# Kernel optimization log

Measured on AMD Instinct MI355X. Metric: run time of the kernel, lower is better.

Reference implementation:

```python
import jax, jax.numpy as jnp
import numpy as np

B, S, VOCAB, P, K, R = 64, 512, 50000, 300, 50, 5


def setup_inputs() -> dict:
    key = jax.random.key(0)
    k0, k1, k2, k3, k4, k5, k6 = jax.random.split(key, 7)
    idx = jax.random.randint(k0, (B, S), 0, VOCAB)
    emb = jax.random.normal(k1, (VOCAB, P), dtype=jnp.float32) * 0.02
    emb = emb.at[0].set(0.0)  # padding_idx=0 row is zero
    C = jax.random.normal(k2, (K, P), dtype=jnp.float32)  # label embeddings ~ N(0,1)
    conv_w = jax.random.normal(k3, (1, 1, 1, 2 * R + 1), dtype=jnp.float32) * 0.1
    conv_b = jax.random.normal(k4, (1,), dtype=jnp.float32) * 0.1
    W2 = jax.random.normal(k5, (K, P), dtype=jnp.float32) / np.sqrt(P).astype(np.float32)
    b2 = jax.random.normal(k6, (K,), dtype=jnp.float32) * 0.01
    return {"idx": idx, "emb": emb, "C": C, "conv_w": conv_w, "conv_b": conv_b, "W2": W2, "b2": b2}


def reference(idx, emb, C, conv_w, conv_b, W2, b2):
    # Embed sentence: [B, S, P]
    x = emb[idx]
    # Cosine label attention
    x_hat = x / (jnp.linalg.norm(x, axis=2, keepdims=True) + 0.001)
    l_hat = C / (jnp.linalg.norm(C, axis=1, keepdims=True) + 0.001)
    G_hat = jnp.einsum('kp,bsp->bks', l_hat, x_hat)  # [B, K, S]
    # Pad seq dim by R on both sides, then conv2d(1->1, kernel (1, 2R+1))
    G_pad = jnp.pad(G_hat, ((0, 0), (0, 0), (R, R)))
    m = jax.lax.conv_general_dilated(
        G_pad[:, None, :, :], conv_w, window_strides=(1, 1), padding='VALID',
        dimension_numbers=('NCHW', 'OIHW', 'NCHW'))[:, 0] + conv_b[0]  # [B, K, S]
    m = jax.nn.relu(m)
    m = jnp.max(m, axis=1)  # max over labels -> [B, S]
    beta = jax.nn.softmax(m, axis=1)[..., None]  # [B, S, 1]
    pooled = jnp.mean(beta * x, axis=1)  # [B, P]
    # Dropout is identity in eval mode; final linear P -> K
    return pooled @ W2.T + b2
```

## Files before the change

### kernel.cpp

```cpp
#include <hip/hip_runtime.h>

#define B_   64
#define S_   512
#define P_   300
#define K_   50
#define MPAD 64
#define LDX  344
#define NS   48
#define SCH  32
#define LDM  67

typedef short short8v __attribute__((ext_vector_type(8)));
typedef float float4v __attribute__((ext_vector_type(4)));

__device__ __forceinline__ short f2bf(float f) {
  unsigned u = __builtin_bit_cast(unsigned, f);
  u = (u + 0x7FFFu + ((u >> 16) & 1u)) >> 16;
  return (short)u;
}
__device__ __forceinline__ float bf2f(short h) {
  return __builtin_bit_cast(float, ((unsigned)(unsigned short)h) << 16);
}

__global__ __launch_bounds__(64) void k1_prep(const float* __restrict__ C,
                                              const float* __restrict__ W2,
                                              short* __restrict__ apack) {
  int bid = blockIdx.x;
  int mat = bid / 40;
  int rem = bid - mat * 40;
  int mt  = rem / 10;
  int ks  = rem - mt * 10;
  int lane = threadIdx.x;
  __shared__ float invn[16];
  if (mat == 0) {
    int rl = lane >> 2, q = lane & 3;
    int m = mt * 16 + rl;
    float ss = 0.f;
    if (m < K_) {
      for (int p = q; p < P_; p += 4) { float v = C[m * P_ + p]; ss += v * v; }
    }
    ss += __shfl_xor(ss, 1);
    ss += __shfl_xor(ss, 2);
    if (q == 0) invn[rl] = 1.f / (sqrtf(ss) + 0.001f);
  }
  __syncthreads();
  int ml = lane & 15, quad = lane >> 4;
  int m = mt * 16 + ml;
  const float* src = (mat == 0) ? C : W2;
  short8v v8;
  #pragma unroll
  for (int j = 0; j < 8; ++j) {
    int k = ks * 32 + quad * 8 + j;
    float v = 0.f;
    if (m < K_ && k < P_) {
      v = src[m * P_ + k];
      if (mat == 0) v *= invn[ml];
    }
    v8[j] = f2bf(v);
  }
  *(short8v*)(apack + (size_t)(((mat * 4 + mt) * 10 + ks) * 512 + lane * 8)) = v8;
}

__global__ __launch_bounds__(256, 3) void k2_gemm(const int* __restrict__ idx,
                                                  const float* __restrict__ emb,
                                                  const short* __restrict__ apack,
                                                  short* __restrict__ Yt,
                                                  const float* __restrict__ conv_w,
                                                  const float* __restrict__ conv_b,
                                                  float* __restrict__ mbuf) {
  __shared__ __align__(16) char smem_raw[NS * LDX * 2];
  __shared__ float scale_s[NS];
  __shared__ float mpart[8][SCH];
  short (*xt)[LDX] = (short(*)[LDX])smem_raw;
  float (*gst)[LDM] = (float(*)[LDM])smem_raw;

  int bid = blockIdx.x;
  int b = bid >> 4, s0 = (bid & 15) * SCH;
  int tid = threadIdx.x;
  int lane = tid & 63;
  int wu = __builtin_amdgcn_readfirstlane(tid >> 6);

  int rows[12];
  #pragma unroll
  for (int r = 0; r < 12; ++r) {
    int sg = s0 - 8 + wu * 12 + r;
    int sgc = sg < 0 ? 0 : (sg >= S_ ? S_ - 1 : sg);
    rows[r] = idx[b * S_ + sgc];
  }

  float ssr[12];
  #pragma unroll
  for (int h = 0; h < 2; ++h) {
    float4 va[6], vb[6];
    #pragma unroll
    for (int r = 0; r < 6; ++r) {
      const float4* src = (const float4*)(emb + (size_t)rows[h * 6 + r] * P_);
      va[r] = src[lane];
      if (lane < 11) vb[r] = src[64 + lane];
    }
    #pragma unroll
    for (int r = 0; r < 6; ++r) {
      int ls = wu * 12 + h * 6 + r;
      int sg = s0 - 8 + ls;
      bool oob = (sg < 0) || (sg >= S_);
      float4 v = va[r];
      if (oob) { v.x = 0.f; v.y = 0.f; v.z = 0.f; v.w = 0.f; }
      float ss = v.x * v.x + v.y * v.y + v.z * v.z + v.w * v.w;
      short4 hh; hh.x = f2bf(v.x); hh.y = f2bf(v.y); hh.z = f2bf(v.z); hh.w = f2bf(v.w);
      *(short4*)&xt[ls][4 * lane] = hh;
      if (lane < 11) {
        float4 v2 = vb[r];
        if (oob) { v2.x = 0.f; v2.y = 0.f; v2.z = 0.f; v2.w = 0.f; }
        ss += v2.x * v2.x + v2.y * v2.y + v2.z * v2.z + v2.w * v2.w;
        short4 h2; h2.x = f2bf(v2.x); h2.y = f2bf(v2.y); h2.z = f2bf(v2.z); h2.w = f2bf(v2.w);
        *(short4*)&xt[ls][256 + 4 * lane] = h2;
      } else if (lane < 16) {
        short4 z = {0, 0, 0, 0};
        *(short4*)&xt[ls][300 + 4 * (lane - 11)] = z;
      }
      ssr[h * 6 + r] = ss;
    }
  }
  #pragma unroll
  for (int r = 0; r < 12; ++r) {
    float ss = ssr[r];
    #pragma unroll
    for (int off = 32; off > 0; off >>= 1) ss += __shfl_xor(ss, off);
    if (lane == 0) scale_s[wu * 12 + r] = 1.f / (sqrtf(ss) + 0.001f);
  }

  const short8v* a1p = (const short8v*)(apack) + (size_t)((0 * 4 + wu) * 10) * 64 + lane;
  const short8v* a2p = (const short8v*)(apack) + (size_t)((1 * 4 + wu) * 10) * 64 + lane;
  short8v a1f[10], a2f[10];
  #pragma unroll
  for (int ks = 0; ks < 10; ++ks) { a1f[ks] = a1p[ks * 64]; a2f[ks] = a2p[ks * 64]; }

  __syncthreads();

  float4v accG[3] = {};
  float4v accY[2] = {};
  int ml = lane & 15, quad = lane >> 4;
  #pragma unroll
  for (int ks = 0; ks < 10; ++ks) {
    int kk = ks * 32 + quad * 8;
    #pragma unroll
    for (int nt = 0; nt < 3; ++nt) {
      short8v bg = *(const short8v*)&xt[nt * 16 + ml][kk];
      accG[nt] = __builtin_amdgcn_mfma_f32_16x16x32_bf16(a1f[ks], bg, accG[nt], 0, 0, 0);
    }
    #pragma unroll
    for (int nt = 0; nt < 2; ++nt) {
      short8v by = *(const short8v*)&xt[8 + nt * 16 + ml][kk];
      accY[nt] = __builtin_amdgcn_mfma_f32_16x16x32_bf16(a2f[ks], by, accY[nt], 0, 0, 0);
    }
  }

  #pragma unroll
  for (int nt = 0; nt < 2; ++nt) {
    int sg = s0 + nt * 16 + ml;
    #pragma unroll
    for (int reg = 0; reg < 4; ++reg) {
      int m = wu * 16 + quad * 4 + reg;
      if (m < K_) Yt[(size_t)(b * MPAD + m) * S_ + sg] = f2bf(accY[nt][reg]);
    }
  }

  float wvv[11];
  #pragma unroll
  for (int t = 0; t < 11; ++t) wvv[t] = conv_w[t];
  float cb = conv_b[0];

  __syncthreads();

  #pragma unroll
  for (int nt = 0; nt < 3; ++nt) {
    int scol = nt * 16 + ml;
    float sc = scale_s[scol];
    #pragma unroll
    for (int reg = 0; reg < 4; ++reg) {
      int m = wu * 16 + quad * 4 + reg;
      gst[scol][m] = accG[nt][reg] * sc;
    }
  }
  __syncthreads();

  int sl = tid & 31, kg = tid >> 5;
  float part = 0.f;
  for (int k = kg; k < K_; k += 8) {
    float acc = cb;
    #pragma unroll
    for (int t = 0; t < 11; ++t) acc += wvv[t] * gst[sl + 3 + t][k];
    part = fmaxf(part, fmaxf(acc, 0.f));
  }
  mpart[kg][sl] = part;
  __syncthreads();
  if (tid < SCH) {
    float m0 = mpart[0][tid];
    #pragma unroll
    for (int i = 1; i < 8; ++i) m0 = fmaxf(m0, mpart[i][tid]);
    mbuf[b * S_ + s0 + tid] = m0;
  }
}

__global__ __launch_bounds__(512) void k3_pool(const float* __restrict__ mbuf,
                                               const short* __restrict__ Yt,
                                               const float* __restrict__ b2,
                                               float* __restrict__ out) {
  __shared__ float beta[S_];
  __shared__ float red[8];
  int b = blockIdx.x;
  int tid = threadIdx.x;
  int lane = tid & 63, wv = tid >> 6;

  float mx = mbuf[b * S_ + tid];

  float r = mx;
  #pragma unroll
  for (int off = 32; off > 0; off >>= 1) r = fmaxf(r, __shfl_xor(r, off));
  if (lane == 0) red[wv] = r;
  __syncthreads();
  float bm = red[0];
  #pragma unroll
  for (int i = 1; i < 8; ++i) bm = fmaxf(bm, red[i]);
  float e = __expf(mx - bm);
  r = e;
  #pragma unroll
  for (int off = 32; off > 0; off >>= 1) r += __shfl_xor(r, off);
  __syncthreads();
  if (lane == 0) red[wv] = r;
  __syncthreads();
  float sum = 0.f;
  #pragma unroll
  for (int i = 0; i < 8; ++i) sum += red[i];
  beta[tid] = e / (sum * (float)S_);
  __syncthreads();

  for (int k = wv; k < K_; k += 8) {
    short8v y = *(const short8v*)(Yt + (((size_t)(b * MPAD + k)) << 9) + lane * 8);
    const float4* bp = (const float4*)&beta[lane * 8];
    float4 b0 = bp[0], b1 = bp[1];
    float acc = b0.x * bf2f(y[0]) + b0.y * bf2f(y[1]) +
                b0.z * bf2f(y[2]) + b0.w * bf2f(y[3]) +
                b1.x * bf2f(y[4]) + b1.y * bf2f(y[5]) +
                b1.z * bf2f(y[6]) + b1.w * bf2f(y[7]);
    #pragma unroll
    for (int off = 32; off > 0; off >>= 1) acc += __shfl_xor(acc, off);
    if (lane == 0) out[b * K_ + k] = acc + b2[k];
  }
}

extern "C" void kernel_launch(void* const* d_in, const int* in_sizes, int n_in,
                              void* d_out, int out_size, void* d_ws, size_t ws_size,
                              hipStream_t stream) {
  const int*   idx    = (const int*)  d_in[0];
  const float* emb    = (const float*)d_in[1];
  const float* C      = (const float*)d_in[2];
  const float* conv_w = (const float*)d_in[3];
  const float* conv_b = (const float*)d_in[4];
  const float* W2     = (const float*)d_in[5];
  const float* b2     = (const float*)d_in[6];
  float* out = (float*)d_out;

  char* ws = (char*)d_ws;
  short* apack = (short*)(ws);
  short* Yt    = (short*)(ws + 81920);
  float* mbuf  = (float*)(ws + 81920 + 4194304);

  hipLaunchKernelGGL(k1_prep, dim3(80),   dim3(64),  0, stream, C, W2, apack);
  hipLaunchKernelGGL(k2_gemm, dim3(1024), dim3(256), 0, stream,
                     idx, emb, apack, Yt, conv_w, conv_b, mbuf);
  hipLaunchKernelGGL(k3_pool, dim3(64),   dim3(512), 0, stream, mbuf, Yt, b2, out);
}
```

Baseline: 142.9 us.

## Fuse pooling kernel into GEMM via last-block atomic counter; raise occupancy

Drops the separate softmax/pooling kernel. Each batch row now has an atomic counter, reset in the prep kernel, and the last of its 16 GEMM blocks to finish computes the softmax and the weighted pooling, which saves a kernel launch and its dependency gap. Launch bounds go from 3 to 4 blocks per SM, and A-fragments are loaded inside the k-loop instead of being preloaded, to cut register pressure. The risks are more global-load latency inside the MFMA loop and a serialized tail on the last block of each batch row.

```diff
diff --git a/kernel.cpp b/kernel.cpp
--- a/kernel.cpp
+++ b/kernel.cpp
@@ -24,13 +24,15 @@
 
 __global__ __launch_bounds__(64) void k1_prep(const float* __restrict__ C,
                                               const float* __restrict__ W2,
-                                              short* __restrict__ apack) {
+                                              short* __restrict__ apack,
+                                              unsigned* __restrict__ cnt) {
   int bid = blockIdx.x;
+  int lane = threadIdx.x;
+  if (bid == 0) cnt[lane] = 0u;
   int mat = bid / 40;
   int rem = bid - mat * 40;
   int mt  = rem / 10;
   int ks  = rem - mt * 10;
-  int lane = threadIdx.x;
   __shared__ float invn[16];
   if (mat == 0) {
     int rl = lane >> 2, q = lane & 3;
@@ -61,16 +63,21 @@
   *(short8v*)(apack + (size_t)(((mat * 4 + mt) * 10 + ks) * 512 + lane * 8)) = v8;
 }
 
-__global__ __launch_bounds__(256, 3) void k2_gemm(const int* __restrict__ idx,
+__global__ __launch_bounds__(256, 4) void k2_gemm(const int* __restrict__ idx,
                                                   const float* __restrict__ emb,
                                                   const short* __restrict__ apack,
                                                   short* __restrict__ Yt,
                                                   const float* __restrict__ conv_w,
                                                   const float* __restrict__ conv_b,
-                                                  float* __restrict__ mbuf) {
+                                                  float* __restrict__ mbuf,
+                                                  const float* __restrict__ b2,
+                                                  float* __restrict__ out,
+                                                  unsigned* __restrict__ cnt) {
   __shared__ __align__(16) char smem_raw[NS * LDX * 2];
   __shared__ float scale_s[NS];
   __shared__ float mpart[8][SCH];
+  __shared__ float redf[4];
+  __shared__ int last_s;
   short (*xt)[LDX] = (short(*)[LDX])smem_raw;
   float (*gst)[LDM] = (float(*)[LDM])smem_raw;
 
@@ -128,30 +135,27 @@
     for (int off = 32; off > 0; off >>= 1) ss += __shfl_xor(ss, off);
     if (lane == 0) scale_s[wu * 12 + r] = 1.f / (sqrtf(ss) + 0.001f);
   }
-
-  const short8v* a1p = (const short8v*)(apack) + (size_t)((0 * 4 + wu) * 10) * 64 + lane;
-  const short8v* a2p = (const short8v*)(apack) + (size_t)((1 * 4 + wu) * 10) * 64 + lane;
-  short8v a1f[10], a2f[10];
-  #pragma unroll
-  for (int ks = 0; ks < 10; ++ks) { a1f[ks] = a1p[ks * 64]; a2f[ks] = a2p[ks * 64]; }
-
   __syncthreads();
 
   float4v accG[3] = {};
   float4v accY[2] = {};
   int ml = lane & 15, quad = lane >> 4;
+  const short8v* a1p = (const short8v*)(apack) + (size_t)((0 * 4 + wu) * 10) * 64 + lane;
+  const short8v* a2p = (const short8v*)(apack) + (size_t)((1 * 4 + wu) * 10) * 64 + lane;
   #pragma unroll
   for (int ks = 0; ks < 10; ++ks) {
+    short8v a1 = a1p[ks * 64];
+    short8v a2 = a2p[ks * 64];
     int kk = ks * 32 + quad * 8;
     #pragma unroll
     for (int nt = 0; nt < 3; ++nt) {
       short8v bg = *(const short8v*)&xt[nt * 16 + ml][kk];
-      accG[nt] = __builtin_amdgcn_mfma_f32_16x16x32_bf16(a1f[ks], bg, accG[nt], 0, 0, 0);
+      accG[nt] = __builtin_amdgcn_mfma_f32_16x16x32_bf16(a1, bg, accG[nt], 0, 0, 0);
     }
     #pragma unroll
     for (int nt = 0; nt < 2; ++nt) {
       short8v by = *(const short8v*)&xt[8 + nt * 16 + ml][kk];
-      accY[nt] = __builtin_amdgcn_mfma_f32_16x16x32_bf16(a2f[ks], by, accY[nt], 0, 0, 0);
+      accY[nt] = __builtin_amdgcn_mfma_f32_16x16x32_bf16(a2, by, accY[nt], 0, 0, 0);
     }
   }
 
@@ -200,49 +204,48 @@
     for (int i = 1; i < 8; ++i) m0 = fmaxf(m0, mpart[i][tid]);
     mbuf[b * S_ + s0 + tid] = m0;
   }
-}
-
-__global__ __launch_bounds__(512) void k3_pool(const float* __restrict__ mbuf,
-                                               const short* __restrict__ Yt,
-                                               const float* __restrict__ b2,
-                                               float* __restrict__ out) {
-  __shared__ float beta[S_];
-  __shared__ float red[8];
-  int b = blockIdx.x;
-  int tid = threadIdx.x;
-  int lane = tid & 63, wv = tid >> 6;
-
-  float mx = mbuf[b * S_ + tid];
-
+  __syncthreads();
+  __threadfence();
+  if (tid == 0) {
+    unsigned old = atomicAdd(&cnt[b], 1u);
+    last_s = (old == 15u);
+  }
+  __syncthreads();
+  if (!last_s) return;
+
+  __threadfence();
+  float* beta = (float*)smem_raw;
+  int wv = tid >> 6;
+
+  float m0 = mbuf[b * S_ + tid];
+  float m1 = mbuf[b * S_ + 256 + tid];
+  float mx = fmaxf(m0, m1);
   float r = mx;
   #pragma unroll
   for (int off = 32; off > 0; off >>= 1) r = fmaxf(r, __shfl_xor(r, off));
-  if (lane == 0) red[wv] = r;
-  __syncthreads();
-  float bm = red[0];
-  #pragma unroll
-  for (int i = 1; i < 8; ++i) bm = fmaxf(bm, red[i]);
-  float e = __expf(mx - bm);
-  r = e;
+  if (lane == 0) redf[wv] = r;
+  __syncthreads();
+  float bm = fmaxf(fmaxf(redf[0], redf[1]), fmaxf(redf[2], redf[3]));
+  float e0 = __expf(m0 - bm), e1 = __expf(m1 - bm);
+  r = e0 + e1;
   #pragma unroll
   for (int off = 32; off > 0; off >>= 1) r += __shfl_xor(r, off);
   __syncthreads();
-  if (lane == 0) red[wv] = r;
-  __syncthreads();
-  float sum = 0.f;
-  #pragma unroll
-  for (int i = 0; i < 8; ++i) sum += red[i];
-  beta[tid] = e / (sum * (float)S_);
-  __syncthreads();
-
-  for (int k = wv; k < K_; k += 8) {
+  if (lane == 0) redf[wv] = r;
+  __syncthreads();
+  float inv = 1.f / ((redf[0] + redf[1] + redf[2] + redf[3]) * (float)S_);
+  beta[tid] = e0 * inv;
+  beta[tid + 256] = e1 * inv;
+  __syncthreads();
+
+  float4 bb0 = *(const float4*)&beta[lane * 8];
+  float4 bb1 = *(const float4*)&beta[lane * 8 + 4];
+  for (int k = wv; k < K_; k += 4) {
     short8v y = *(const short8v*)(Yt + (((size_t)(b * MPAD + k)) << 9) + lane * 8);
-    const float4* bp = (const float4*)&beta[lane * 8];
-    float4 b0 = bp[0], b1 = bp[1];
-    float acc = b0.x * bf2f(y[0]) + b0.y * bf2f(y[1]) +
-                b0.z * bf2f(y[2]) + b0.w * bf2f(y[3]) +
-                b1.x * bf2f(y[4]) + b1.y * bf2f(y[5]) +
-                b1.z * bf2f(y[6]) + b1.w * bf2f(y[7]);
+    float acc = bb0.x * bf2f(y[0]) + bb0.y * bf2f(y[1]) +
+                bb0.z * bf2f(y[2]) + bb0.w * bf2f(y[3]) +
+                bb1.x * bf2f(y[4]) + bb1.y * bf2f(y[5]) +
+                bb1.z * bf2f(y[6]) + bb1.w * bf2f(y[7]);
     #pragma unroll
     for (int off = 32; off > 0; off >>= 1) acc += __shfl_xor(acc, off);
     if (lane == 0) out[b * K_ + k] = acc + b2[k];
@@ -262,12 +265,12 @@
   float* out = (float*)d_out;
 
   char* ws = (char*)d_ws;
-  short* apack = (short*)(ws);
-  short* Yt    = (short*)(ws + 81920);
-  float* mbuf  = (float*)(ws + 81920 + 4194304);
-
-  hipLaunchKernelGGL(k1_prep, dim3(80),   dim3(64),  0, stream, C, W2, apack);
+  short*    apack = (short*)(ws);
+  short*    Yt    = (short*)(ws + 81920);
+  float*    mbuf  = (float*)(ws + 81920 + 4194304);
+  unsigned* cnt   = (unsigned*)(ws + 81920 + 4194304 + 131072);
+
+  hipLaunchKernelGGL(k1_prep, dim3(80),   dim3(64),  0, stream, C, W2, apack, cnt);
   hipLaunchKernelGGL(k2_gemm, dim3(1024), dim3(256), 0, stream,
-                     idx, emb, apack, Yt, conv_w, conv_b, mbuf);
-  hipLaunchKernelGGL(k3_pool, dim3(64),   dim3(512), 0, stream, mbuf, Yt, b2, out);
-}
+                     idx, emb, apack, Yt, conv_w, conv_b, mbuf, b2, out, cnt);
+}
```

After: 245.1 us. 1.71x slower.

## Stage embedding rows via direct global-to-LDS loads and split pooling across more blocks

Applied to the files above, without the earlier changes.

The gather of embedding rows in the GEMM kernel now uses global_load_lds DMA straight into shared memory as fp32. The rows are then converted in place to bf16 with packed conversion instructions, and the row norms are computed from LDS. This removes the register round-trip on the gather and lets the A-fragment loads overlap with it. The cost is a larger LDS footprint, so occupancy drops from 3 to 2 blocks per CU. The pooling kernel is also split four ways over labels, giving 256 blocks, and beta is hoisted out of the label loop; each block now recomputes the softmax.

```diff
diff --git a/kernel.cpp b/kernel.cpp
--- a/kernel.cpp
+++ b/kernel.cpp
@@ -5,21 +5,31 @@
 #define P_   300
 #define K_   50
 #define MPAD 64
-#define LDX  344
 #define NS   48
 #define SCH  32
+#define LDB  1232
 #define LDM  67
 
 typedef short short8v __attribute__((ext_vector_type(8)));
 typedef float float4v __attribute__((ext_vector_type(4)));
 
+__device__ __forceinline__ float bf2f(short h) {
+  return __builtin_bit_cast(float, ((unsigned)(unsigned short)h) << 16);
+}
 __device__ __forceinline__ short f2bf(float f) {
   unsigned u = __builtin_bit_cast(unsigned, f);
   u = (u + 0x7FFFu + ((u >> 16) & 1u)) >> 16;
   return (short)u;
 }
-__device__ __forceinline__ float bf2f(short h) {
-  return __builtin_bit_cast(float, ((unsigned)(unsigned short)h) << 16);
+__device__ __forceinline__ unsigned cvtpk(float lo, float hi) {
+  unsigned r;
+  asm("v_cvt_pk_bf16_f32 %0, %1, %2" : "=v"(r) : "v"(lo), "v"(hi));
+  return r;
+}
+__device__ __forceinline__ void dma16(const float* g, void* l) {
+  __builtin_amdgcn_global_load_lds(
+      (const __attribute__((address_space(1))) void*)g,
+      (__attribute__((address_space(3))) void*)l, 16, 0, 0);
 }
 
 __global__ __launch_bounds__(64) void k1_prep(const float* __restrict__ C,
@@ -61,17 +71,16 @@
   *(short8v*)(apack + (size_t)(((mat * 4 + mt) * 10 + ks) * 512 + lane * 8)) = v8;
 }
 
-__global__ __launch_bounds__(256, 3) void k2_gemm(const int* __restrict__ idx,
+__global__ __launch_bounds__(256, 2) void k2_gemm(const int* __restrict__ idx,
                                                   const float* __restrict__ emb,
                                                   const short* __restrict__ apack,
                                                   short* __restrict__ Yt,
                                                   const float* __restrict__ conv_w,
                                                   const float* __restrict__ conv_b,
                                                   float* __restrict__ mbuf) {
-  __shared__ __align__(16) char smem_raw[NS * LDX * 2];
+  __shared__ __align__(16) char smem_raw[NS * LDB];
   __shared__ float scale_s[NS];
   __shared__ float mpart[8][SCH];
-  short (*xt)[LDX] = (short(*)[LDX])smem_raw;
   float (*gst)[LDM] = (float(*)[LDM])smem_raw;
 
   int bid = blockIdx.x;
@@ -88,45 +97,16 @@
     rows[r] = idx[b * S_ + sgc];
   }
 
-  float ssr[12];
-  #pragma unroll
-  for (int h = 0; h < 2; ++h) {
-    float4 va[6], vb[6];
-    #pragma unroll
-    for (int r = 0; r < 6; ++r) {
-      const float4* src = (const float4*)(emb + (size_t)rows[h * 6 + r] * P_);
-      va[r] = src[lane];
-      if (lane < 11) vb[r] = src[64 + lane];
-    }
-    #pragma unroll
-    for (int r = 0; r < 6; ++r) {
-      int ls = wu * 12 + h * 6 + r;
-      int sg = s0 - 8 + ls;
-      bool oob = (sg < 0) || (sg >= S_);
-      float4 v = va[r];
-      if (oob) { v.x = 0.f; v.y = 0.f; v.z = 0.f; v.w = 0.f; }
-      float ss = v.x * v.x + v.y * v.y + v.z * v.z + v.w * v.w;
-      short4 hh; hh.x = f2bf(v.x); hh.y = f2bf(v.y); hh.z = f2bf(v.z); hh.w = f2bf(v.w);
-      *(short4*)&xt[ls][4 * lane] = hh;
-      if (lane < 11) {
-        float4 v2 = vb[r];
-        if (oob) { v2.x = 0.f; v2.y = 0.f; v2.z = 0.f; v2.w = 0.f; }
-        ss += v2.x * v2.x + v2.y * v2.y + v2.z * v2.z + v2.w * v2.w;
-        short4 h2; h2.x = f2bf(v2.x); h2.y = f2bf(v2.y); h2.z = f2bf(v2.z); h2.w = f2bf(v2.w);
-        *(short4*)&xt[ls][256 + 4 * lane] = h2;
-      } else if (lane < 16) {
-        short4 z = {0, 0, 0, 0};
-        *(short4*)&xt[ls][300 + 4 * (lane - 11)] = z;
-      }
-      ssr[h * 6 + r] = ss;
-    }
-  }
   #pragma unroll
   for (int r = 0; r < 12; ++r) {
-    float ss = ssr[r];
-    #pragma unroll
-    for (int off = 32; off > 0; off >>= 1) ss += __shfl_xor(ss, off);
-    if (lane == 0) scale_s[wu * 12 + r] = 1.f / (sqrtf(ss) + 0.001f);
+    int ls = wu * 12 + r;
+    int sg = s0 - 8 + ls;
+    if (sg >= 0 && sg < S_) {
+      const float* src = emb + (size_t)rows[r] * P_;
+      char* dst = smem_raw + ls * LDB;
+      dma16(src + 4 * lane, dst);
+      dma16(src + 44 + 4 * lane, dst + 176);
+    }
   }
 
   const short8v* a1p = (const short8v*)(apack) + (size_t)((0 * 4 + wu) * 10) * 64 + lane;
@@ -135,6 +115,35 @@
   #pragma unroll
   for (int ks = 0; ks < 10; ++ks) { a1f[ks] = a1p[ks * 64]; a2f[ks] = a2p[ks * 64]; }
 
+  asm volatile("s_waitcnt vmcnt(0)" ::: "memory");
+
+  #pragma unroll
+  for (int r = 0; r < 12; ++r) {
+    int ls = wu * 12 + r;
+    int sg = s0 - 8 + ls;
+    char* rowp = smem_raw + ls * LDB;
+    float ss = 0.f;
+    if (sg >= 0 && sg < S_) {
+      float4 va = *(const float4*)(rowp + 16 * lane);
+      float4 vb = {0.f, 0.f, 0.f, 0.f};
+      if (lane < 11) vb = *(const float4*)(rowp + 1024 + 16 * lane);
+      ss = va.x * va.x + va.y * va.y + va.z * va.z + va.w * va.w +
+           vb.x * vb.x + vb.y * vb.y + vb.z * vb.z + vb.w * vb.w;
+      unsigned u0 = cvtpk(va.x, va.y), u1 = cvtpk(va.z, va.w);
+      *(uint2*)(rowp + 8 * lane) = make_uint2(u0, u1);
+      if (lane < 11) {
+        unsigned u2 = cvtpk(vb.x, vb.y), u3 = cvtpk(vb.z, vb.w);
+        *(uint2*)(rowp + 512 + 8 * lane) = make_uint2(u2, u3);
+      }
+      if (lane < 5) *(uint2*)(rowp + 600 + 8 * lane) = make_uint2(0u, 0u);
+    } else {
+      *(uint2*)(rowp + 8 * lane) = make_uint2(0u, 0u);
+      if (lane < 16) *(uint2*)(rowp + 512 + 8 * lane) = make_uint2(0u, 0u);
+    }
+    #pragma unroll
+    for (int off = 32; off > 0; off >>= 1) ss += __shfl_xor(ss, off);
+    if (lane == 0) scale_s[ls] = 1.f / (sqrtf(ss) + 0.001f);
+  }
   __syncthreads();
 
   float4v accG[3] = {};
@@ -142,15 +151,15 @@
   int ml = lane & 15, quad = lane >> 4;
   #pragma unroll
   for (int ks = 0; ks < 10; ++ks) {
-    int kk = ks * 32 + quad * 8;
+    int kb = (ks * 32 + quad * 8) * 2;
     #pragma unroll
     for (int nt = 0; nt < 3; ++nt) {
-      short8v bg = *(const short8v*)&xt[nt * 16 + ml][kk];
+      short8v bg = *(const short8v*)(smem_raw + (nt * 16 + ml) * LDB + kb);
       accG[nt] = __builtin_amdgcn_mfma_f32_16x16x32_bf16(a1f[ks], bg, accG[nt], 0, 0, 0);
     }
     #pragma unroll
     for (int nt = 0; nt < 2; ++nt) {
-      short8v by = *(const short8v*)&xt[8 + nt * 16 + ml][kk];
+      short8v by = *(const short8v*)(smem_raw + (8 + nt * 16 + ml) * LDB + kb);
       accY[nt] = __builtin_amdgcn_mfma_f32_16x16x32_bf16(a2f[ks], by, accY[nt], 0, 0, 0);
     }
   }
@@ -208,7 +217,7 @@
                                                float* __restrict__ out) {
   __shared__ float beta[S_];
   __shared__ float red[8];
-  int b = blockIdx.x;
+  int b = blockIdx.x >> 2, part = blockIdx.x & 3;
   int tid = threadIdx.x;
   int lane = tid & 63, wv = tid >> 6;
 
@@ -235,10 +244,10 @@
   beta[tid] = e / (sum * (float)S_);
   __syncthreads();
 
-  for (int k = wv; k < K_; k += 8) {
+  const float4* bp = (const float4*)&beta[lane * 8];
+  float4 b0 = bp[0], b1 = bp[1];
+  for (int k = part + 4 * wv; k < K_; k += 32) {
     short8v y = *(const short8v*)(Yt + (((size_t)(b * MPAD + k)) << 9) + lane * 8);
-    const float4* bp = (const float4*)&beta[lane * 8];
-    float4 b0 = bp[0], b1 = bp[1];
     float acc = b0.x * bf2f(y[0]) + b0.y * bf2f(y[1]) +
                 b0.z * bf2f(y[2]) + b0.w * bf2f(y[3]) +
                 b1.x * bf2f(y[4]) + b1.y * bf2f(y[5]) +
@@ -269,5 +278,5 @@
   hipLaunchKernelGGL(k1_prep, dim3(80),   dim3(64),  0, stream, C, W2, apack);
   hipLaunchKernelGGL(k2_gemm, dim3(1024), dim3(256), 0, stream,
                      idx, emb, apack, Yt, conv_w, conv_b, mbuf);
-  hipLaunchKernelGGL(k3_pool, dim3(64),   dim3(512), 0, stream, mbuf, Yt, b2, out);
-}
+  hipLaunchKernelGGL(k3_pool, dim3(256),  dim3(512), 0, stream, mbuf, Yt, b2, out);
+}
```

Result: slower. 150.2 us (+5.1%).
